# Kernel tuning notes

Hardware: AMD Instinct MI355X
Metric: run time of the kernel (lower is better)

The kernel has to match this reference:

```python
import jax, jax.numpy as jnp
import numpy as np


def setup_inputs() -> dict:
    key = jax.random.key(0)
    k1, k2 = jax.random.split(key)
    # positive inputs -> positive matmul outputs, so log is well-defined
    x = jax.random.uniform(k1, (8, 2048, 1024), dtype=jnp.float32)
    matrix = jax.random.uniform(k2, (1024, 1024), dtype=jnp.float32)
    return {"x": x, "matrix": matrix}


def reference(x, matrix):
    # mm_big: shifted quantized matmul; mm_small: no-shift quantized matmul.
    # In float math both compute the same product (quantization differs only
    # in fixed-point scaling), so we compute it once; XLA would CSE anyway.
    y_big = jnp.einsum('bsk,km->bsm', x, matrix)    # [B,S,M]
    y_small = jnp.einsum('bsk,km->bsm', x, matrix)  # NoShiftMM, same float math

    big = (y_big > 0).astype(x.dtype)   # gt0
    small = 1.0 - big                   # oplus(neg(big)) = 1 + (-big)

    eps = jnp.finfo(x.dtype).tiny
    # AddIdentityTLUT(torch.log): LUT approximation of log; float reference is log.
    z_big = jnp.log(jnp.maximum(y_big, eps)) * big      # lut_big -> mul_big
    z_small = jnp.log(jnp.maximum(y_small, eps)) * small  # lut_small -> mul_small
    return z_big + z_small  # add_output
```

## Files before the change

kernel.cpp:

```cpp
#include <hip/hip_runtime.h>
#include <cstdint>
#include <cstddef>

#define M_GLOB 16384
#define N_GLOB 1024
#define K_GLOB 1024

#define BM 256
#define BN 128
#define BKF 128

typedef unsigned char  u8;
typedef unsigned short u16;
typedef __attribute__((ext_vector_type(4))) float  f32x4;
typedef __attribute__((ext_vector_type(16))) float f32x16;
typedef __attribute__((ext_vector_type(4))) unsigned int  u32x4;
typedef __attribute__((ext_vector_type(2))) unsigned int  u32x2;
typedef __attribute__((ext_vector_type(8))) int  i32x8;
typedef __attribute__((ext_vector_type(8))) __bf16 bf16x8;

static __device__ __forceinline__ unsigned pack2_bf16(float lo, float hi) {
    unsigned bl = __builtin_bit_cast(unsigned, lo);
    unsigned bh = __builtin_bit_cast(unsigned, hi);
    return (bh & 0xFFFF0000u) | (bl >> 16);
}

static __device__ __forceinline__ unsigned cvt4_fp8(float a, float b, float c, float d) {
    int w = __builtin_amdgcn_cvt_pk_fp8_f32(a, b, 0, false);
    w = __builtin_amdgcn_cvt_pk_fp8_f32(c, d, w, true);
    return (unsigned)w;
}

static __device__ __forceinline__ void barrier_raw() {
    asm volatile("s_barrier" ::: "memory");
}

__global__ __launch_bounds__(256)
void prep_fp8_kernel(const float* __restrict__ A, u8* __restrict__ Ab,
                     const float* __restrict__ B, u8* __restrict__ Bt, int nA) {
    __shared__ float tile[32][33];
    const int tid = threadIdx.x;
    if ((int)blockIdx.x < nA) {
        const size_t i = ((size_t)blockIdx.x * 256 + tid) * 16;
        f32x4 f0 = *(const f32x4*)(A + i);
        f32x4 f1 = *(const f32x4*)(A + i + 4);
        f32x4 f2 = *(const f32x4*)(A + i + 8);
        f32x4 f3 = *(const f32x4*)(A + i + 12);
        u32x4 o;
        o.x = cvt4_fp8(f0.x, f0.y, f0.z, f0.w);
        o.y = cvt4_fp8(f1.x, f1.y, f1.z, f1.w);
        o.z = cvt4_fp8(f2.x, f2.y, f2.z, f2.w);
        o.w = cvt4_fp8(f3.x, f3.y, f3.z, f3.w);
        *(u32x4*)(Ab + i) = o;
    } else {
        const int bid = (int)blockIdx.x - nA;
        const int n0 = (bid & 31) * 32;
        const int k0 = (bid >> 5) * 32;
        const int tx = tid & 31;
        const int ty = tid >> 5;
#pragma unroll
        for (int i = 0; i < 32; i += 8)
            tile[ty + i][tx] = B[(size_t)(k0 + ty + i) * N_GLOB + n0 + tx];
        __syncthreads();
#pragma unroll
        for (int i = 0; i < 32; i += 8) {
            int w = __builtin_amdgcn_cvt_pk_fp8_f32(tile[tx][ty + i], 0.f, 0, false);
            Bt[(size_t)(n0 + ty + i) * K_GLOB + k0 + tx] = (u8)(w & 0xFF);
        }
    }
}

__global__ __launch_bounds__(256, 2)
void gemm_mx_kernel(const u8* __restrict__ A,
                    const u8* __restrict__ Bt,
                    float* __restrict__ C)
{
    __shared__ __attribute__((aligned(16))) char smem[49152];
    float* Cs = (float*)smem;

    const int tid  = threadIdx.x;
    const int wave = tid >> 6;
    const int lane = tid & 63;
    const int wr   = wave >> 1;
    const int wc   = wave & 1;
    const int l32  = lane & 31;
    const int half = lane >> 5;

    const int b    = blockIdx.x;
    const int xcd  = b & 7;
    const int idx  = b >> 3;
    const int m0   = (xcd * 8 + (idx >> 3)) * BM;
    const int n0   = (idx & 7) * BN;

    const int srow = lane >> 3;
    const int sp   = lane & 7;
    const int sc   = sp ^ srow;
    const u8* gA = A  + (size_t)(m0 + srow) * K_GLOB + sc * 16;
    const u8* gB = Bt + (size_t)(n0 + srow) * K_GLOB + sc * 16;

    f32x16 acc[4][2];
#pragma unroll
    for (int i = 0; i < 4; ++i)
#pragma unroll
        for (int j = 0; j < 2; ++j)
#pragma unroll
            for (int r = 0; r < 16; ++r)
                acc[i][j][r] = 0.f;

    const int swz = lane & 7;
    const int scale1 = 0x7F7F7F7F;

    u32x4 ra[8], rb[4];
#pragma unroll
    for (int s = 0; s < 8; ++s)
        ra[s] = *(const u32x4*)(gA + (size_t)((s * 4 + wave) * 8) * K_GLOB);
#pragma unroll
    for (int s = 0; s < 4; ++s)
        rb[s] = *(const u32x4*)(gB + (size_t)((s * 4 + wave) * 8) * K_GLOB);

    for (int kt = 0; kt < K_GLOB / BKF; ++kt) {
#pragma unroll
        for (int s = 0; s < 8; ++s) {
            const int row = (s * 4 + wave) * 8 + srow;
            *(u32x4*)(smem + row * 128 + sp * 16) = ra[s];
        }
#pragma unroll
        for (int s = 0; s < 4; ++s) {
            const int row = (s * 4 + wave) * 8 + srow;
            *(u32x4*)(smem + 32768 + row * 128 + sp * 16) = rb[s];
        }
        __syncthreads();

        if (kt + 1 < K_GLOB / BKF) {
            const size_t k1 = (size_t)(kt + 1) * BKF;
#pragma unroll
            for (int s = 0; s < 8; ++s)
                ra[s] = *(const u32x4*)(gA + (size_t)((s * 4 + wave) * 8) * K_GLOB + k1);
#pragma unroll
            for (int s = 0; s < 4; ++s)
                rb[s] = *(const u32x4*)(gB + (size_t)((s * 4 + wave) * 8) * K_GLOB + k1);
        }

#pragma unroll
        for (int s = 0; s < 2; ++s) {
            const int c0 = s * 4 + half * 2;
            const int p0 = ((c0    ) ^ swz) * 16;
            const int p1 = ((c0 + 1) ^ swz) * 16;
            i32x8 af[4], bf[2];
#pragma unroll
            for (int i = 0; i < 4; ++i) {
                const int row = wr * 128 + i * 32 + l32;
                u32x4 lo = *(const u32x4*)(smem + row * 128 + p0);
                u32x4 hi = *(const u32x4*)(smem + row * 128 + p1);
                af[i][0] = lo.x; af[i][1] = lo.y; af[i][2] = lo.z; af[i][3] = lo.w;
                af[i][4] = hi.x; af[i][5] = hi.y; af[i][6] = hi.z; af[i][7] = hi.w;
            }
#pragma unroll
            for (int j = 0; j < 2; ++j) {
                const int row = wc * 64 + j * 32 + l32;
                u32x4 lo = *(const u32x4*)(smem + 32768 + row * 128 + p0);
                u32x4 hi = *(const u32x4*)(smem + 32768 + row * 128 + p1);
                bf[j][0] = lo.x; bf[j][1] = lo.y; bf[j][2] = lo.z; bf[j][3] = lo.w;
                bf[j][4] = hi.x; bf[j][5] = hi.y; bf[j][6] = hi.z; bf[j][7] = hi.w;
            }
#pragma unroll
            for (int i = 0; i < 4; ++i)
#pragma unroll
                for (int j = 0; j < 2; ++j)
                    acc[i][j] = __builtin_amdgcn_mfma_scale_f32_32x32x64_f8f6f4(
                        af[i], bf[j], acc[i][j],
                        0 , 0 ,
                        0, scale1, 0, scale1);
        }
        barrier_raw();
    }

    const float LN2 = 0.69314718055994530942f;
    const int c4 = tid & 31;
    const int r0 = tid >> 5;
#pragma unroll
    for (int h = 0; h < 4; ++h) {
        __syncthreads();
        if (wr == (h >> 1)) {
#pragma unroll
            for (int ii = 0; ii < 2; ++ii) {
                const int i = (h & 1) * 2 + ii;
#pragma unroll
                for (int j = 0; j < 2; ++j) {
                    const int col = wc * 64 + j * 32 + l32;
#pragma unroll
                    for (int r = 0; r < 16; ++r) {
                        const int row32 = (r & 3) + 8 * (r >> 2) + 4 * half;
                        float v = fmaxf(acc[i][j][r], 1.17549435e-38f);
                        Cs[(ii * 32 + row32) * 132 + col] = __log2f(v) * LN2;
                    }
                }
            }
        }
        __syncthreads();
#pragma unroll
        for (int s2 = 0; s2 < 8; ++s2) {
            const int row = s2 * 8 + r0;
            f32x4 v = *(const f32x4*)&Cs[row * 132 + c4 * 4];
            __builtin_nontemporal_store(v,
                (f32x4*)&C[(size_t)(m0 + h * 64 + row) * N_GLOB + n0 + c4 * 4]);
        }
    }
}

#define FBM 128
#define FBN 128
#define LDK 40
__global__ __launch_bounds__(256)
void logmm_fused_kernel(const float* __restrict__ A,
                        const float* __restrict__ Bf,
                        float* __restrict__ C)
{
    __shared__ u16 As[FBM][LDK];
    __shared__ u16 Bs[FBN][LDK];

    const int tid  = threadIdx.x;
    const int lane = tid & 63;
    const int wave = tid >> 6;
    const int wr   = wave >> 1;
    const int wc   = wave & 1;
    const int quad = lane >> 4;
    const int l16  = lane & 15;

    const int m0 = blockIdx.y * FBM;
    const int n0 = blockIdx.x * FBN;

    f32x4 acc[4][4];
#pragma unroll
    for (int i = 0; i < 4; ++i)
#pragma unroll
        for (int j = 0; j < 4; ++j)
            acc[i][j] = f32x4{0.f, 0.f, 0.f, 0.f};

    const int ga_row = tid >> 2;
    const int ga_c8  = (tid & 3) * 8;
    const int fb_nt = tid >> 3;
    const int fb_kt = tid & 7;

    for (int kt = 0; kt < K_GLOB / 32; ++kt) {
        const int k0 = kt * 32;
#pragma unroll
        for (int s = 0; s < 2; ++s) {
            const int row = ga_row + s * 64;
            const float* src = A + (size_t)(m0 + row) * K_GLOB + k0 + ga_c8;
            f32x4 f0 = *(const f32x4*)src;
            f32x4 f1 = *(const f32x4*)(src + 4);
            u32x4 o;
            o.x = pack2_bf16(f0.x, f0.y);
            o.y = pack2_bf16(f0.z, f0.w);
            o.z = pack2_bf16(f1.x, f1.y);
            o.w = pack2_bf16(f1.z, f1.w);
            *(u32x4*)&As[row][ga_c8] = o;
        }
        {
            f32x4 r0 = *(const f32x4*)(Bf + (size_t)(k0 + fb_kt * 4 + 0) * N_GLOB + n0 + fb_nt * 4);
            f32x4 r1 = *(const f32x4*)(Bf + (size_t)(k0 + fb_kt * 4 + 1) * N_GLOB + n0 + fb_nt * 4);
            f32x4 r2 = *(const f32x4*)(Bf + (size_t)(k0 + fb_kt * 4 + 2) * N_GLOB + n0 + fb_nt * 4);
            f32x4 r3 = *(const f32x4*)(Bf + (size_t)(k0 + fb_kt * 4 + 3) * N_GLOB + n0 + fb_nt * 4);
#pragma unroll
            for (int j = 0; j < 4; ++j) {
                u32x2 o;
                o.x = pack2_bf16(r0[j], r1[j]);
                o.y = pack2_bf16(r2[j], r3[j]);
                *(u32x2*)&Bs[fb_nt * 4 + j][fb_kt * 4] = o;
            }
        }

        __syncthreads();

        bf16x8 af[4], bfr[4];
#pragma unroll
        for (int i = 0; i < 4; ++i)
            af[i] = __builtin_bit_cast(bf16x8, *(const u32x4*)&As[wr * 64 + i * 16 + l16][quad * 8]);
#pragma unroll
        for (int j = 0; j < 4; ++j)
            bfr[j] = __builtin_bit_cast(bf16x8, *(const u32x4*)&Bs[wc * 64 + j * 16 + l16][quad * 8]);

#pragma unroll
        for (int i = 0; i < 4; ++i)
#pragma unroll
            for (int j = 0; j < 4; ++j)
                acc[i][j] = __builtin_amdgcn_mfma_f32_16x16x32_bf16(af[i], bfr[j], acc[i][j], 0, 0, 0);

        __syncthreads();
    }

    const float LN2 = 0.69314718055994530942f;
#pragma unroll
    for (int i = 0; i < 4; ++i) {
#pragma unroll
        for (int j = 0; j < 4; ++j) {
            const int col = n0 + wc * 64 + j * 16 + l16;
#pragma unroll
            for (int r = 0; r < 4; ++r) {
                const int row = m0 + wr * 64 + i * 16 + quad * 4 + r;
                float v = fmaxf(acc[i][j][r], 1.17549435e-38f);
                C[(size_t)row * N_GLOB + col] = __log2f(v) * LN2;
            }
        }
    }
}

extern "C" void kernel_launch(void* const* d_in, const int* in_sizes, int n_in,
                              void* d_out, int out_size, void* d_ws, size_t ws_size,
                              hipStream_t stream) {
    const float* A = (const float*)d_in[0];
    const float* B = (const float*)d_in[1];
    float* C = (float*)d_out;

    const size_t bt_bytes = (size_t)N_GLOB * K_GLOB;
    const size_t ab_bytes = (size_t)M_GLOB * K_GLOB;
    const int nA = (M_GLOB * K_GLOB) / (256 * 16);

    if (ws_size >= bt_bytes + ab_bytes) {
        u8* Bt = (u8*)d_ws;
        u8* Ab = (u8*)d_ws + bt_bytes;
        prep_fp8_kernel<<<nA + 1024, 256, 0, stream>>>(A, Ab, B, Bt, nA);
        gemm_mx_kernel<<<(M_GLOB / BM) * (N_GLOB / BN), 256, 0, stream>>>(Ab, Bt, C);
    } else {
        logmm_fused_kernel<<<dim3(N_GLOB / FBN, M_GLOB / FBM), 256, 0, stream>>>(A, B, C);
    }
}
```

Baseline: 132.4 us.

## Fuse fp32-to-fp8 conversion of A into GEMM mainloop, halve M tile

```diff
diff --git a/kernel.cpp b/kernel.cpp
--- a/kernel.cpp
+++ b/kernel.cpp
@@ -6,7 +6,7 @@
 #define N_GLOB 1024
 #define K_GLOB 1024
 
-#define BM 256
+#define BM 128
 #define BN 128
 #define BKF 128
 
@@ -36,46 +36,31 @@
 }
 
 __global__ __launch_bounds__(256)
-void prep_fp8_kernel(const float* __restrict__ A, u8* __restrict__ Ab,
-                     const float* __restrict__ B, u8* __restrict__ Bt, int nA) {
+void prep_b_kernel(const float* __restrict__ B, u8* __restrict__ Bt) {
     __shared__ float tile[32][33];
     const int tid = threadIdx.x;
-    if ((int)blockIdx.x < nA) {
-        const size_t i = ((size_t)blockIdx.x * 256 + tid) * 16;
-        f32x4 f0 = *(const f32x4*)(A + i);
-        f32x4 f1 = *(const f32x4*)(A + i + 4);
-        f32x4 f2 = *(const f32x4*)(A + i + 8);
-        f32x4 f3 = *(const f32x4*)(A + i + 12);
-        u32x4 o;
-        o.x = cvt4_fp8(f0.x, f0.y, f0.z, f0.w);
-        o.y = cvt4_fp8(f1.x, f1.y, f1.z, f1.w);
-        o.z = cvt4_fp8(f2.x, f2.y, f2.z, f2.w);
-        o.w = cvt4_fp8(f3.x, f3.y, f3.z, f3.w);
-        *(u32x4*)(Ab + i) = o;
-    } else {
-        const int bid = (int)blockIdx.x - nA;
-        const int n0 = (bid & 31) * 32;
-        const int k0 = (bid >> 5) * 32;
-        const int tx = tid & 31;
-        const int ty = tid >> 5;
-#pragma unroll
-        for (int i = 0; i < 32; i += 8)
-            tile[ty + i][tx] = B[(size_t)(k0 + ty + i) * N_GLOB + n0 + tx];
-        __syncthreads();
-#pragma unroll
-        for (int i = 0; i < 32; i += 8) {
-            int w = __builtin_amdgcn_cvt_pk_fp8_f32(tile[tx][ty + i], 0.f, 0, false);
-            Bt[(size_t)(n0 + ty + i) * K_GLOB + k0 + tx] = (u8)(w & 0xFF);
-        }
+    const int bid = (int)blockIdx.x;
+    const int n0 = (bid & 31) * 32;
+    const int k0 = (bid >> 5) * 32;
+    const int tx = tid & 31;
+    const int ty = tid >> 5;
+#pragma unroll
+    for (int i = 0; i < 32; i += 8)
+        tile[ty + i][tx] = B[(size_t)(k0 + ty + i) * N_GLOB + n0 + tx];
+    __syncthreads();
+#pragma unroll
+    for (int i = 0; i < 32; i += 8) {
+        int w = __builtin_amdgcn_cvt_pk_fp8_f32(tile[tx][ty + i], 0.f, 0, false);
+        Bt[(size_t)(n0 + ty + i) * K_GLOB + k0 + tx] = (u8)(w & 0xFF);
     }
 }
 
 __global__ __launch_bounds__(256, 2)
-void gemm_mx_kernel(const u8* __restrict__ A,
-                    const u8* __restrict__ Bt,
-                    float* __restrict__ C)
+void gemm_fused_kernel(const float* __restrict__ A,
+                       const u8* __restrict__ Bt,
+                       float* __restrict__ C)
 {
-    __shared__ __attribute__((aligned(16))) char smem[49152];
+    __shared__ __attribute__((aligned(16))) char smem[32768];
     float* Cs = (float*)smem;
 
     const int tid  = threadIdx.x;
@@ -86,21 +71,26 @@
     const int l32  = lane & 31;
     const int half = lane >> 5;
 
-    const int b    = blockIdx.x;
+    const int b    = (int)blockIdx.x;
     const int xcd  = b & 7;
     const int idx  = b >> 3;
-    const int m0   = (xcd * 8 + (idx >> 3)) * BM;
+    const int m0   = (xcd * 16 + (idx >> 3)) * BM;
     const int n0   = (idx & 7) * BN;
 
     const int srow = lane >> 3;
     const int sp   = lane & 7;
     const int sc   = sp ^ srow;
-    const u8* gA = A  + (size_t)(m0 + srow) * K_GLOB + sc * 16;
     const u8* gB = Bt + (size_t)(n0 + srow) * K_GLOB + sc * 16;
 
-    f32x16 acc[4][2];
-#pragma unroll
-    for (int i = 0; i < 4; ++i)
+    const int t4 = tid >> 4;
+    const int tl = tid & 15;
+    const float* gA = A + (size_t)(m0 + t4) * K_GLOB + tl * 8;
+    const int zA = t4 & 7;
+    const int ldsA_cst = (((tl >> 1) ^ zA) << 4) + (tl & 1) * 8;
+
+    f32x16 acc[2][2];
+#pragma unroll
+    for (int i = 0; i < 2; ++i)
 #pragma unroll
         for (int j = 0; j < 2; ++j)
 #pragma unroll
@@ -110,32 +100,46 @@
     const int swz = lane & 7;
     const int scale1 = 0x7F7F7F7F;
 
-    u32x4 ra[8], rb[4];
-#pragma unroll
-    for (int s = 0; s < 8; ++s)
-        ra[s] = *(const u32x4*)(gA + (size_t)((s * 4 + wave) * 8) * K_GLOB);
+    u32x2 sA[8];
+    u32x4 rb[4];
+
+    {
+        f32x4 f0[8], f1[8];
+#pragma unroll
+        for (int s = 0; s < 8; ++s) {
+            f0[s] = *(const f32x4*)(gA + (size_t)s * 16 * K_GLOB);
+            f1[s] = *(const f32x4*)(gA + (size_t)s * 16 * K_GLOB + 4);
+        }
+#pragma unroll
+        for (int s = 0; s < 8; ++s) {
+            sA[s].x = cvt4_fp8(f0[s].x, f0[s].y, f0[s].z, f0[s].w);
+            sA[s].y = cvt4_fp8(f1[s].x, f1[s].y, f1[s].z, f1[s].w);
+        }
+    }
 #pragma unroll
     for (int s = 0; s < 4; ++s)
         rb[s] = *(const u32x4*)(gB + (size_t)((s * 4 + wave) * 8) * K_GLOB);
 
     for (int kt = 0; kt < K_GLOB / BKF; ++kt) {
 #pragma unroll
-        for (int s = 0; s < 8; ++s) {
-            const int row = (s * 4 + wave) * 8 + srow;
-            *(u32x4*)(smem + row * 128 + sp * 16) = ra[s];
-        }
+        for (int s = 0; s < 8; ++s)
+            *(u32x2*)(smem + (s * 16 + t4) * 128 + ldsA_cst) = sA[s];
 #pragma unroll
         for (int s = 0; s < 4; ++s) {
             const int row = (s * 4 + wave) * 8 + srow;
-            *(u32x4*)(smem + 32768 + row * 128 + sp * 16) = rb[s];
-        }
-        __syncthreads();
-
-        if (kt + 1 < K_GLOB / BKF) {
+            *(u32x4*)(smem + 16384 + row * 128 + sp * 16) = rb[s];
+        }
+        __syncthreads();
+
+        f32x4 f0[8], f1[8];
+        const bool more = (kt + 1 < K_GLOB / BKF);
+        if (more) {
             const size_t k1 = (size_t)(kt + 1) * BKF;
 #pragma unroll
-            for (int s = 0; s < 8; ++s)
-                ra[s] = *(const u32x4*)(gA + (size_t)((s * 4 + wave) * 8) * K_GLOB + k1);
+            for (int s = 0; s < 8; ++s) {
+                f0[s] = *(const f32x4*)(gA + k1 + (size_t)s * 16 * K_GLOB);
+                f1[s] = *(const f32x4*)(gA + k1 + (size_t)s * 16 * K_GLOB + 4);
+            }
 #pragma unroll
             for (int s = 0; s < 4; ++s)
                 rb[s] = *(const u32x4*)(gB + (size_t)((s * 4 + wave) * 8) * K_GLOB + k1);
@@ -146,10 +150,10 @@
             const int c0 = s * 4 + half * 2;
             const int p0 = ((c0    ) ^ swz) * 16;
             const int p1 = ((c0 + 1) ^ swz) * 16;
-            i32x8 af[4], bf[2];
-#pragma unroll
-            for (int i = 0; i < 4; ++i) {
-                const int row = wr * 128 + i * 32 + l32;
+            i32x8 af[2], bf[2];
+#pragma unroll
+            for (int i = 0; i < 2; ++i) {
+                const int row = wr * 64 + i * 32 + l32;
                 u32x4 lo = *(const u32x4*)(smem + row * 128 + p0);
                 u32x4 hi = *(const u32x4*)(smem + row * 128 + p1);
                 af[i][0] = lo.x; af[i][1] = lo.y; af[i][2] = lo.z; af[i][3] = lo.w;
@@ -158,13 +162,13 @@
 #pragma unroll
             for (int j = 0; j < 2; ++j) {
                 const int row = wc * 64 + j * 32 + l32;
-                u32x4 lo = *(const u32x4*)(smem + 32768 + row * 128 + p0);
-                u32x4 hi = *(const u32x4*)(smem + 32768 + row * 128 + p1);
+                u32x4 lo = *(const u32x4*)(smem + 16384 + row * 128 + p0);
+                u32x4 hi = *(const u32x4*)(smem + 16384 + row * 128 + p1);
                 bf[j][0] = lo.x; bf[j][1] = lo.y; bf[j][2] = lo.z; bf[j][3] = lo.w;
                 bf[j][4] = hi.x; bf[j][5] = hi.y; bf[j][6] = hi.z; bf[j][7] = hi.w;
             }
 #pragma unroll
-            for (int i = 0; i < 4; ++i)
+            for (int i = 0; i < 2; ++i)
 #pragma unroll
                 for (int j = 0; j < 2; ++j)
                     acc[i][j] = __builtin_amdgcn_mfma_scale_f32_32x32x64_f8f6f4(
@@ -172,6 +176,14 @@
                         0 , 0 ,
                         0, scale1, 0, scale1);
         }
+
+        if (more) {
+#pragma unroll
+            for (int s = 0; s < 8; ++s) {
+                sA[s].x = cvt4_fp8(f0[s].x, f0[s].y, f0[s].z, f0[s].w);
+                sA[s].y = cvt4_fp8(f1[s].x, f1[s].y, f1[s].z, f1[s].w);
+            }
+        }
         barrier_raw();
     }
 
@@ -182,28 +194,25 @@
     for (int h = 0; h < 4; ++h) {
         __syncthreads();
         if (wr == (h >> 1)) {
-#pragma unroll
-            for (int ii = 0; ii < 2; ++ii) {
-                const int i = (h & 1) * 2 + ii;
-#pragma unroll
-                for (int j = 0; j < 2; ++j) {
-                    const int col = wc * 64 + j * 32 + l32;
-#pragma unroll
-                    for (int r = 0; r < 16; ++r) {
-                        const int row32 = (r & 3) + 8 * (r >> 2) + 4 * half;
-                        float v = fmaxf(acc[i][j][r], 1.17549435e-38f);
-                        Cs[(ii * 32 + row32) * 132 + col] = __log2f(v) * LN2;
-                    }
+            const int i = h & 1;
+#pragma unroll
+            for (int j = 0; j < 2; ++j) {
+                const int col = wc * 64 + j * 32 + l32;
+#pragma unroll
+                for (int r = 0; r < 16; ++r) {
+                    const int row32 = (r & 3) + 8 * (r >> 2) + 4 * half;
+                    float v = fmaxf(acc[i][j][r], 1.17549435e-38f);
+                    Cs[row32 * 132 + col] = __log2f(v) * LN2;
                 }
             }
         }
         __syncthreads();
 #pragma unroll
-        for (int s2 = 0; s2 < 8; ++s2) {
+        for (int s2 = 0; s2 < 4; ++s2) {
             const int row = s2 * 8 + r0;
             f32x4 v = *(const f32x4*)&Cs[row * 132 + c4 * 4];
             __builtin_nontemporal_store(v,
-                (f32x4*)&C[(size_t)(m0 + h * 64 + row) * N_GLOB + n0 + c4 * 4]);
+                (f32x4*)&C[(size_t)(m0 + h * 32 + row) * N_GLOB + n0 + c4 * 4]);
         }
     }
 }
@@ -314,14 +323,11 @@
     float* C = (float*)d_out;
 
     const size_t bt_bytes = (size_t)N_GLOB * K_GLOB;
-    const size_t ab_bytes = (size_t)M_GLOB * K_GLOB;
-    const int nA = (M_GLOB * K_GLOB) / (256 * 16);
-
-    if (ws_size >= bt_bytes + ab_bytes) {
+
+    if (ws_size >= bt_bytes) {
         u8* Bt = (u8*)d_ws;
-        u8* Ab = (u8*)d_ws + bt_bytes;
-        prep_fp8_kernel<<<nA + 1024, 256, 0, stream>>>(A, Ab, B, Bt, nA);
-        gemm_mx_kernel<<<(M_GLOB / BM) * (N_GLOB / BN), 256, 0, stream>>>(Ab, Bt, C);
+        prep_b_kernel<<<1024, 256, 0, stream>>>(B, Bt);
+        gemm_fused_kernel<<<(M_GLOB / BM) * (N_GLOB / BN), 256, 0, stream>>>(A, Bt, C);
     } else {
         logmm_fused_kernel<<<dim3(N_GLOB / FBN, M_GLOB / FBM), 256, 0, stream>>>(A, B, C);
     }
```

Measured after the change: 155.2 us. 17.2% more time.

## Shrink GEMM tile to 128x128 and load tiles via direct global-to-LDS

Applied to the files above, without the earlier changes.

```diff
diff --git a/kernel.cpp b/kernel.cpp
--- a/kernel.cpp
+++ b/kernel.cpp
@@ -6,7 +6,7 @@
 #define N_GLOB 1024
 #define K_GLOB 1024
 
-#define BM 256
+#define BM 128
 #define BN 128
 #define BKF 128
 
@@ -31,8 +31,11 @@
     return (unsigned)w;
 }
 
-static __device__ __forceinline__ void barrier_raw() {
-    asm volatile("s_barrier" ::: "memory");
+static __device__ __forceinline__ void gload_lds16(const u8* g, char* l) {
+    __builtin_amdgcn_global_load_lds(
+        (const __attribute__((address_space(1))) unsigned int*)g,
+        (__attribute__((address_space(3))) unsigned int*)l,
+        16, 0, 0);
 }
 
 __global__ __launch_bounds__(256)
@@ -70,12 +73,12 @@
     }
 }
 
-__global__ __launch_bounds__(256, 2)
+__global__ __launch_bounds__(256, 3)
 void gemm_mx_kernel(const u8* __restrict__ A,
                     const u8* __restrict__ Bt,
                     float* __restrict__ C)
 {
-    __shared__ __attribute__((aligned(16))) char smem[49152];
+    __shared__ __attribute__((aligned(16))) char smem[32768];
     float* Cs = (float*)smem;
 
     const int tid  = threadIdx.x;
@@ -86,10 +89,10 @@
     const int l32  = lane & 31;
     const int half = lane >> 5;
 
-    const int b    = blockIdx.x;
+    const int b    = (int)blockIdx.x;
     const int xcd  = b & 7;
     const int idx  = b >> 3;
-    const int m0   = (xcd * 8 + (idx >> 3)) * BM;
+    const int m0   = (xcd * 16 + (idx >> 3)) * BM;
     const int n0   = (idx & 7) * BN;
 
     const int srow = lane >> 3;
@@ -97,10 +100,12 @@
     const int sc   = sp ^ srow;
     const u8* gA = A  + (size_t)(m0 + srow) * K_GLOB + sc * 16;
     const u8* gB = Bt + (size_t)(n0 + srow) * K_GLOB + sc * 16;
-
-    f32x16 acc[4][2];
-#pragma unroll
-    for (int i = 0; i < 4; ++i)
+    char* ldsA = smem + wave * 1024;
+    char* ldsB = smem + 16384 + wave * 1024;
+
+    f32x16 acc[2][2];
+#pragma unroll
+    for (int i = 0; i < 2; ++i)
 #pragma unroll
         for (int j = 0; j < 2; ++j)
 #pragma unroll
@@ -110,46 +115,27 @@
     const int swz = lane & 7;
     const int scale1 = 0x7F7F7F7F;
 
-    u32x4 ra[8], rb[4];
-#pragma unroll
-    for (int s = 0; s < 8; ++s)
-        ra[s] = *(const u32x4*)(gA + (size_t)((s * 4 + wave) * 8) * K_GLOB);
-#pragma unroll
-    for (int s = 0; s < 4; ++s)
-        rb[s] = *(const u32x4*)(gB + (size_t)((s * 4 + wave) * 8) * K_GLOB);
-
     for (int kt = 0; kt < K_GLOB / BKF; ++kt) {
-#pragma unroll
-        for (int s = 0; s < 8; ++s) {
-            const int row = (s * 4 + wave) * 8 + srow;
-            *(u32x4*)(smem + row * 128 + sp * 16) = ra[s];
-        }
-#pragma unroll
-        for (int s = 0; s < 4; ++s) {
-            const int row = (s * 4 + wave) * 8 + srow;
-            *(u32x4*)(smem + 32768 + row * 128 + sp * 16) = rb[s];
-        }
-        __syncthreads();
-
-        if (kt + 1 < K_GLOB / BKF) {
-            const size_t k1 = (size_t)(kt + 1) * BKF;
-#pragma unroll
-            for (int s = 0; s < 8; ++s)
-                ra[s] = *(const u32x4*)(gA + (size_t)((s * 4 + wave) * 8) * K_GLOB + k1);
-#pragma unroll
-            for (int s = 0; s < 4; ++s)
-                rb[s] = *(const u32x4*)(gB + (size_t)((s * 4 + wave) * 8) * K_GLOB + k1);
-        }
+        const int ko = kt * BKF;
+#pragma unroll
+        for (int s = 0; s < 4; ++s)
+            gload_lds16(gA + (size_t)(s * 4 + wave) * 8 * K_GLOB + ko,
+                        ldsA + s * 4096);
+#pragma unroll
+        for (int s = 0; s < 4; ++s)
+            gload_lds16(gB + (size_t)(s * 4 + wave) * 8 * K_GLOB + ko,
+                        ldsB + s * 4096);
+        __syncthreads();
 
 #pragma unroll
         for (int s = 0; s < 2; ++s) {
             const int c0 = s * 4 + half * 2;
             const int p0 = ((c0    ) ^ swz) * 16;
             const int p1 = ((c0 + 1) ^ swz) * 16;
-            i32x8 af[4], bf[2];
-#pragma unroll
-            for (int i = 0; i < 4; ++i) {
-                const int row = wr * 128 + i * 32 + l32;
+            i32x8 af[2], bf[2];
+#pragma unroll
+            for (int i = 0; i < 2; ++i) {
+                const int row = wr * 64 + i * 32 + l32;
                 u32x4 lo = *(const u32x4*)(smem + row * 128 + p0);
                 u32x4 hi = *(const u32x4*)(smem + row * 128 + p1);
                 af[i][0] = lo.x; af[i][1] = lo.y; af[i][2] = lo.z; af[i][3] = lo.w;
@@ -158,13 +144,13 @@
 #pragma unroll
             for (int j = 0; j < 2; ++j) {
                 const int row = wc * 64 + j * 32 + l32;
-                u32x4 lo = *(const u32x4*)(smem + 32768 + row * 128 + p0);
-                u32x4 hi = *(const u32x4*)(smem + 32768 + row * 128 + p1);
+                u32x4 lo = *(const u32x4*)(smem + 16384 + row * 128 + p0);
+                u32x4 hi = *(const u32x4*)(smem + 16384 + row * 128 + p1);
                 bf[j][0] = lo.x; bf[j][1] = lo.y; bf[j][2] = lo.z; bf[j][3] = lo.w;
                 bf[j][4] = hi.x; bf[j][5] = hi.y; bf[j][6] = hi.z; bf[j][7] = hi.w;
             }
 #pragma unroll
-            for (int i = 0; i < 4; ++i)
+            for (int i = 0; i < 2; ++i)
 #pragma unroll
                 for (int j = 0; j < 2; ++j)
                     acc[i][j] = __builtin_amdgcn_mfma_scale_f32_32x32x64_f8f6f4(
@@ -172,7 +158,7 @@
                         0 , 0 ,
                         0, scale1, 0, scale1);
         }
-        barrier_raw();
+        __syncthreads();
     }
 
     const float LN2 = 0.69314718055994530942f;
@@ -182,28 +168,25 @@
     for (int h = 0; h < 4; ++h) {
         __syncthreads();
         if (wr == (h >> 1)) {
-#pragma unroll
-            for (int ii = 0; ii < 2; ++ii) {
-                const int i = (h & 1) * 2 + ii;
-#pragma unroll
-                for (int j = 0; j < 2; ++j) {
-                    const int col = wc * 64 + j * 32 + l32;
-#pragma unroll
-                    for (int r = 0; r < 16; ++r) {
-                        const int row32 = (r & 3) + 8 * (r >> 2) + 4 * half;
-                        float v = fmaxf(acc[i][j][r], 1.17549435e-38f);
-                        Cs[(ii * 32 + row32) * 132 + col] = __log2f(v) * LN2;
-                    }
+            const int i = h & 1;
+#pragma unroll
+            for (int j = 0; j < 2; ++j) {
+                const int col = wc * 64 + j * 32 + l32;
+#pragma unroll
+                for (int r = 0; r < 16; ++r) {
+                    const int row32 = (r & 3) + 8 * (r >> 2) + 4 * half;
+                    float v = fmaxf(acc[i][j][r], 1.17549435e-38f);
+                    Cs[row32 * 132 + col] = __log2f(v) * LN2;
                 }
             }
         }
         __syncthreads();
 #pragma unroll
-        for (int s2 = 0; s2 < 8; ++s2) {
+        for (int s2 = 0; s2 < 4; ++s2) {
             const int row = s2 * 8 + r0;
             f32x4 v = *(const f32x4*)&Cs[row * 132 + c4 * 4];
             __builtin_nontemporal_store(v,
-                (f32x4*)&C[(size_t)(m0 + h * 64 + row) * N_GLOB + n0 + c4 * 4]);
+                (f32x4*)&C[(size_t)(m0 + h * 32 + row) * N_GLOB + n0 + c4 * 4]);
         }
     }
 }
```

Result: no change. 132.5 us (+0.1%).
